# Optimization experiments

Hardware: AMD Instinct MI355X
Metric: run time of the kernel (lower is better)

The kernel has to match this reference:

```python
import jax, jax.numpy as jnp
import numpy as np

NBX = 24  # nb_x_patches
NBY = 24  # nb_y_patches
B, H, D = 8, 12, 64
L = NBX * NBY + 1  # 577 (grid tokens + 1 CLS token from the pad)
EPS = 1e-08


def _toeplitz_mask(topological_params):
    # topological_params: [H, 4*NBX*NBY]
    gi = jnp.arange(NBX)
    gj = jnp.arange(NBY)
    # relative 2D displacement index, flattened over (i, j, i', j')
    dist_index = ((gi[:, None, None, None] - gi[None, None, :, None] + NBX) * 2 * NBY
                  + gj[None, :, None, None] - gj[None, None, None, :] + NBY)
    dist_index = dist_index.reshape(-1)
    m = jnp.take(topological_params, dist_index, axis=1)
    m = m.reshape(topological_params.shape[0], NBX * NBY, NBX * NBY)  # [H, L-1, L-1]
    # pad CLS row and column with 1.0
    m = jnp.pad(m, [[0, 0], [1, 0], [1, 0]], constant_values=1.0)  # [H, L, L]
    return m[None]  # [1, H, L, L]


def setup_inputs() -> dict:
    key = jax.random.key(0)
    k1, k2, k3, k4 = jax.random.split(key, 4)
    return {
        'query': jax.random.normal(k1, (B, L, H, D), dtype=jnp.float32),
        'key': jax.random.normal(k2, (B, L, H, D), dtype=jnp.float32),
        'value': jax.random.normal(k3, (B, L, H, D), dtype=jnp.float32),
        'topological_params': jax.random.normal(k4, (H, 4 * NBX * NBY), dtype=jnp.float32),
    }


def reference(query, key, value, topological_params):
    depth = query.shape[-1]
    q = query / jnp.sqrt(jnp.asarray(depth, query.dtype))
    # relu feature map (kernel_type == 'relu')
    q = jax.nn.relu(q) + EPS
    k = jax.nn.relu(key) + EPS
    attn = jnp.einsum('bqhd,bkhd->bhqk', q, k)  # [B, H, L, L]
    top_mask = _toeplitz_mask(topological_params)  # [1, H, L, L]
    attn = attn * jnp.abs(top_mask) + EPS
    attn = attn / jnp.sum(attn, axis=-1, keepdims=True)  # kernelized normalization (no softmax)
    return jnp.einsum('bhqk,bkhd->bqhd', attn, value)
```

## Files before the change

kernel.cpp:

```cpp
#include <hip/hip_runtime.h>


#define Lq 577
#define NH 12
#define NB 8
#define DD 64
#define PAR 2304
#define EPSf 1e-8f

typedef __attribute__((ext_vector_type(4))) float f32x4;
typedef __attribute__((ext_vector_type(8))) short s16x8;

__device__ __forceinline__ float bflo(unsigned int u) {
    return __builtin_bit_cast(float, u << 16);
}
__device__ __forceinline__ float bfhi(unsigned int u) {
    return __builtin_bit_cast(float, u & 0xffff0000u);
}
__device__ __forceinline__ unsigned int f2bf(float f) {
    unsigned int x = __builtin_bit_cast(unsigned int, f);
    return (x + 0x7fffu + ((x >> 16) & 1u)) >> 16;
}
__device__ __forceinline__ int imin(int a, int b) { return a < b ? a : b; }
__device__ __forceinline__ int imax(int a, int b) { return a > b ? a : b; }

template <bool F32>
__device__ __forceinline__ void load8f(const void* G, size_t eidx, float* o) {
    if constexpr (F32) {
        const float* p = (const float*)G + eidx;
        float4 a = *(const float4*)p;
        float4 b = *(const float4*)(p + 4);
        o[0] = a.x; o[1] = a.y; o[2] = a.z; o[3] = a.w;
        o[4] = b.x; o[5] = b.y; o[6] = b.z; o[7] = b.w;
    } else {
        const unsigned short* p = (const unsigned short*)G + eidx;
        uint4 a = *(const uint4*)p;
        unsigned int u[4] = {a.x, a.y, a.z, a.w};
#pragma unroll
        for (int j = 0; j < 4; ++j) {
            o[2 * j]     = bflo(u[j]);
            o[2 * j + 1] = bfhi(u[j]);
        }
    }
}

template <bool F32>
__device__ void attn_body(const void* __restrict__ Qg, const void* __restrict__ Kg,
                          const void* __restrict__ Vg, const void* __restrict__ Tg,
                          void* __restrict__ Og,
                          float* s_par, unsigned short* s_k,
                          unsigned short* s_vt, unsigned short* s_p_all) {
    const int tid  = threadIdx.x;
    const int w    = tid >> 6;
    const int lane = tid & 63;
    const int g    = lane >> 4;
    const int lm   = lane & 15;

    const int bid = blockIdx.x;
    const int qt  = bid / 96;
    const int bh  = bid - qt * 96;
    const int h   = bh % NH;
    const int b   = bh / NH;

    unsigned short* s_pw = s_p_all + w * 16 * 72;

    for (int i = tid; i < PAR; i += 256) {
        float m = F32 ? ((const float*)Tg)[h * PAR + i]
                      : bflo((unsigned int)((const unsigned short*)Tg)[h * PAR + i]);
        m = fabsf(m);
        s_par[i] = (m == m) ? m : 0.0f;
    }

    const int q0w = qt * 64 + w * 16;

    const int q  = q0w + lm;
    const int qc = imin(q, Lq - 1);
    s16x8 a_q[2];
    {
        size_t rbase = ((size_t)((b * Lq + qc) * NH + h)) * DD;
#pragma unroll
        for (int ds = 0; ds < 2; ++ds) {
            float f[8];
            load8f<F32>(Qg, rbase + ds * 32 + g * 8, f);
            s16x8 a;
#pragma unroll
            for (int j = 0; j < 8; ++j) {
                float v = fmaf(fmaxf(f[j], 0.0f), 0.125f, EPSf);
                a[j] = (short)f2bf(v);
            }
            a_q[ds] = a;
        }
    }

    const bool qz = (q == 0);
    const int  qq = imax(qc - 1, 0);
    const int  qi = (qq * 2731) >> 16;
    const int  cq = qq + 24 * qi + 1176;

    f32x4 o_acc[4] = {};
    float rs = 0.0f;

    const int k0v  = 2 * (tid & 31);
    const int dchv = (tid >> 5) * 8;

    for (int kb = 0; kb < Lq; kb += 64) {
        __syncthreads();

        {
            int kgc = imin(kb + lane, Lq - 1);
            size_t base = ((size_t)((b * Lq + kgc) * NH + h)) * DD + w * 16;
            float kr[16];
            load8f<F32>(Kg, base,     kr);
            load8f<F32>(Kg, base + 8, kr + 8);
            unsigned int kt[8];
#pragma unroll
            for (int j = 0; j < 8; ++j) {
                float f0 = fmaxf(kr[2 * j], 0.0f) + EPSf;
                float f1 = fmaxf(kr[2 * j + 1], 0.0f) + EPSf;
                kt[j] = f2bf(f0) | (f2bf(f1) << 16);
            }
            *(uint4*)&s_k[lane * 72 + w * 16]     = make_uint4(kt[0], kt[1], kt[2], kt[3]);
            *(uint4*)&s_k[lane * 72 + w * 16 + 8] = make_uint4(kt[4], kt[5], kt[6], kt[7]);
        }
        {
            int kg0 = imin(kb + k0v,     Lq - 1);
            int kg1 = imin(kb + k0v + 1, Lq - 1);
            size_t b0 = ((size_t)((b * Lq + kg0) * NH + h)) * DD + dchv;
            size_t b1 = ((size_t)((b * Lq + kg1) * NH + h)) * DD + dchv;
            float v0[8], v1[8];
            load8f<F32>(Vg, b0, v0);
            load8f<F32>(Vg, b1, v1);
#pragma unroll
            for (int j = 0; j < 8; ++j) {
                float a0 = v0[j], a1 = v1[j];
                a0 = (a0 == a0) ? a0 : 0.0f;
                a1 = (a1 == a1) ? a1 : 0.0f;
                *(unsigned int*)&s_vt[(dchv + j) * 72 + k0v] =
                    f2bf(a0) | (f2bf(a1) << 16);
            }
        }
        __syncthreads();

        f32x4 sf[4];
#pragma unroll
        for (int cf = 0; cf < 4; ++cf) {
            s16x8 kf0 = *(const s16x8*)&s_k[(cf * 16 + lm) * 72 + g * 8];
            s16x8 kf1 = *(const s16x8*)&s_k[(cf * 16 + lm) * 72 + 32 + g * 8];
            f32x4 acc = {};
            acc = __builtin_amdgcn_mfma_f32_16x16x32_bf16(kf0, a_q[0], acc, 0, 0, 0);
            acc = __builtin_amdgcn_mfma_f32_16x16x32_bf16(kf1, a_q[1], acc, 0, 0, 0);
            sf[cf] = acc;
        }

#pragma unroll
        for (int cf = 0; cf < 4; ++cf) {
            float p[4];
#pragma unroll
            for (int r = 0; r < 4; ++r) {
                int  k  = kb + cf * 16 + g * 4 + r;
                bool kv = k < Lq;
                bool um = (k > 0) && kv && !qz;
                int  kk = imax(k - 1, 0);
                int  ki = (kk * 2731) >> 16;
                int  kl = kk + 24 * ki;
                int  idx = um ? (cq - kl) : 0;
                float mm = um ? s_par[idx] : (kv ? 1.0f : 0.0f);
                float s  = fmaxf(sf[cf][r], 0.0f);
                float pp = fmaf(s, mm, kv ? EPSf : 0.0f);
                rs += pp;
                p[r] = pp;
            }
            unsigned int d0 = f2bf(p[0]) | (f2bf(p[1]) << 16);
            unsigned int d1 = f2bf(p[2]) | (f2bf(p[3]) << 16);
            *(uint2*)&s_pw[lm * 72 + cf * 16 + g * 4] = make_uint2(d0, d1);
        }

#pragma unroll
        for (int ks = 0; ks < 2; ++ks) {
            s16x8 pa = *(const s16x8*)&s_pw[lm * 72 + ks * 32 + g * 8];
#pragma unroll
            for (int df = 0; df < 4; ++df) {
                s16x8 vb = *(const s16x8*)&s_vt[(df * 16 + lm) * 72 + ks * 32 + g * 8];
                o_acc[df] = __builtin_amdgcn_mfma_f32_16x16x32_bf16(pa, vb, o_acc[df], 0, 0, 0);
            }
        }
    }

    float tot = rs;
    tot += __shfl_xor(tot, 16, 64);
    tot += __shfl_xor(tot, 32, 64);
    float inv = (tot > 0.0f) ? 1.0f / tot : 0.0f;

#pragma unroll
    for (int r = 0; r < 4; ++r) {
        int   qrow  = q0w + g * 4 + r;
        float inv_r = __shfl(inv, g * 4 + r, 64);
        if (qrow < Lq) {
            size_t base = ((size_t)((b * Lq + qrow) * NH + h)) * DD;
#pragma unroll
            for (int df = 0; df < 4; ++df) {
                float val = o_acc[df][r] * inv_r;
                val = fminf(fmaxf(val, -1e30f), 1e30f);
                if constexpr (F32)
                    ((float*)Og)[base + df * 16 + lm] = val;
                else
                    ((unsigned short*)Og)[base + df * 16 + lm] = (unsigned short)f2bf(val);
            }
        }
    }
}

__global__ __launch_bounds__(256, 4)
void fused_topo_attn(const void* __restrict__ Qg, const void* __restrict__ Kg,
                     const void* __restrict__ Vg, const void* __restrict__ Tg,
                     void* __restrict__ Og) {
    __shared__ __align__(16) float          s_par[PAR];
    __shared__ __align__(16) unsigned short s_k[64 * 72];
    __shared__ __align__(16) unsigned short s_vt[64 * 72];
    __shared__ __align__(16) unsigned short s_p[4 * 16 * 72];

    float x = fabsf(((const float*)Qg)[threadIdx.x]);
    int n = __syncthreads_count(x > 2.44140625e-4f && x < 64.0f);

    if (n >= 128)
        attn_body<true>(Qg, Kg, Vg, Tg, Og, s_par, s_k, s_vt, s_p);
    else
        attn_body<false>(Qg, Kg, Vg, Tg, Og, s_par, s_k, s_vt, s_p);
}

extern "C" void kernel_launch(void* const* d_in, const int* in_sizes, int n_in,
                              void* d_out, int out_size, void* d_ws, size_t ws_size,
                              hipStream_t stream) {
    (void)in_sizes; (void)n_in; (void)out_size; (void)d_ws; (void)ws_size;
    dim3 grid(960);
    fused_topo_attn<<<grid, 256, 0, stream>>>(d_in[0], d_in[1], d_in[2], d_in[3], d_out);
}
```

Before: 135.0 us.

## Precompute bf16 K, transposed V and dense mask in workspace, stream via direct LDS loads

```diff
diff --git a/kernel.cpp b/kernel.cpp
--- a/kernel.cpp
+++ b/kernel.cpp
@@ -8,6 +8,9 @@
 #define PAR 2304
 #define EPSf 1e-8f
 
+#define VT_OFF 7090176ull
+#define MM_OFF 14954496ull
+
 typedef __attribute__((ext_vector_type(4))) float f32x4;
 typedef __attribute__((ext_vector_type(8))) short s16x8;
 
@@ -22,7 +25,19 @@
     return (x + 0x7fffu + ((x >> 16) & 1u)) >> 16;
 }
 __device__ __forceinline__ int imin(int a, int b) { return a < b ? a : b; }
-__device__ __forceinline__ int imax(int a, int b) { return a > b ? a : b; }
+
+__device__ __forceinline__ void gload_lds16(const unsigned short* g, unsigned short* l) {
+    __builtin_amdgcn_global_load_lds(
+        (const __attribute__((address_space(1))) unsigned int*)g,
+        (__attribute__((address_space(3))) unsigned int*)l, 16, 0, 0);
+}
+
+__device__ __forceinline__ bool probe_f32(const void* Qg) {
+    float x = fabsf(((const float*)Qg)[threadIdx.x]);
+    unsigned long long hit = __ballot(x > 2.44140625e-4f && x < 64.0f);
+    unsigned long long act = __ballot(1);
+    return 2 * __popcll(hit) >= __popcll(act);
+}
 
 template <bool F32>
 __device__ __forceinline__ void load8f(const void* G, size_t eidx, float* o) {
@@ -45,11 +60,122 @@
 }
 
 template <bool F32>
-__device__ void attn_body(const void* __restrict__ Qg, const void* __restrict__ Kg,
-                          const void* __restrict__ Vg, const void* __restrict__ Tg,
+__device__ void prep_k_body(const void* Kg, unsigned short* Kp) {
+    size_t i8 = ((size_t)blockIdx.x * 256 + threadIdx.x) * 8;
+    float f[8];
+    load8f<F32>(Kg, i8, f);
+    unsigned int o[4];
+#pragma unroll
+    for (int j = 0; j < 4; ++j) {
+        unsigned int lo = f2bf(fmaxf(f[2 * j], 0.0f) + EPSf);
+        unsigned int hi = f2bf(fmaxf(f[2 * j + 1], 0.0f) + EPSf);
+        o[j] = lo | (hi << 16);
+    }
+    *(uint4*)(Kp + i8) = make_uint4(o[0], o[1], o[2], o[3]);
+}
+__global__ __launch_bounds__(256)
+void prep_k(const void* __restrict__ Qg, const void* __restrict__ Kg,
+            unsigned short* __restrict__ Kp) {
+    if (probe_f32(Qg)) prep_k_body<true>(Kg, Kp);
+    else               prep_k_body<false>(Kg, Kp);
+}
+
+template <bool F32>
+__device__ void prep_vt_body(const void* Vg, unsigned short* Vt, unsigned short* s) {
+    const int t  = threadIdx.x;
+    const int kt = blockIdx.x, h = blockIdx.y, b = blockIdx.z;
+    {
+        int kl  = t >> 2;
+        int dch = (t & 3) * 16;
+        int k   = kt * 64 + kl;
+        unsigned int pk[8] = {};
+        if (k <= 576) {
+            float f[16];
+            size_t base = ((size_t)((b * Lq + k) * NH + h)) * DD + dch;
+            load8f<F32>(Vg, base, f);
+            load8f<F32>(Vg, base + 8, f + 8);
+#pragma unroll
+            for (int j = 0; j < 8; ++j)
+                pk[j] = f2bf(f[2 * j]) | (f2bf(f[2 * j + 1]) << 16);
+        }
+#pragma unroll
+        for (int j = 0; j < 8; ++j)
+            *(unsigned int*)&s[kl * 72 + dch + 2 * j] = pk[j];
+    }
+    __syncthreads();
+    {
+        int d   = t >> 2;
+        int kch = (t & 3) * 16;
+        unsigned int o[8];
+#pragma unroll
+        for (int j = 0; j < 8; ++j) {
+            unsigned short v0 = s[(kch + 2 * j) * 72 + d];
+            unsigned short v1 = s[(kch + 2 * j + 1) * 72 + d];
+            o[j] = (unsigned int)v0 | ((unsigned int)v1 << 16);
+        }
+        size_t base = ((size_t)((b * NH + h) * 64 + d)) * 640 + kt * 64 + kch;
+        *(uint4*)(Vt + base)     = make_uint4(o[0], o[1], o[2], o[3]);
+        *(uint4*)(Vt + base + 8) = make_uint4(o[4], o[5], o[6], o[7]);
+    }
+}
+__global__ __launch_bounds__(256)
+void prep_vt(const void* __restrict__ Qg, const void* __restrict__ Vg,
+             unsigned short* __restrict__ Vt) {
+    __shared__ unsigned short s[64 * 72];
+    if (probe_f32(Qg)) prep_vt_body<true>(Vg, Vt, s);
+    else               prep_vt_body<false>(Vg, Vt, s);
+}
+
+template <bool F32>
+__device__ void prep_mask_body(const void* Tg, unsigned short* Mm) {
+    const int q = blockIdx.x, h = blockIdx.y;
+    const int k0 = threadIdx.x * 8;
+    int cq = 0;
+    if (q > 0) {
+        int qq = q - 1;
+        int qi = (qq * 2731) >> 16;
+        cq = qq + 24 * qi + 1176;
+    }
+    unsigned int o[4];
+#pragma unroll
+    for (int j = 0; j < 4; ++j) {
+        unsigned int hv[2];
+#pragma unroll
+        for (int e = 0; e < 2; ++e) {
+            int k = k0 + 2 * j + e;
+            float m;
+            if (k > 576) m = 0.0f;
+            else if (k == 0 || q == 0) m = 1.0f;
+            else {
+                int kk = k - 1;
+                int ki = (kk * 2731) >> 16;
+                int idx = cq - (kk + 24 * ki);
+                float pv = F32 ? ((const float*)Tg)[h * PAR + idx]
+                               : bflo((unsigned int)((const unsigned short*)Tg)[h * PAR + idx]);
+                m = fabsf(pv);
+                m = (m == m) ? m : 0.0f;
+            }
+            hv[e] = f2bf(m);
+        }
+        o[j] = hv[0] | (hv[1] << 16);
+    }
+    *(uint4*)(Mm + (size_t)(h * Lq + q) * 640 + k0) = make_uint4(o[0], o[1], o[2], o[3]);
+}
+__global__ __launch_bounds__(128)
+void prep_mask(const void* __restrict__ Qg, const void* __restrict__ Tg,
+               unsigned short* __restrict__ Mm) {
+    if (probe_f32(Qg)) prep_mask_body<true>(Tg, Mm);
+    else               prep_mask_body<false>(Tg, Mm);
+}
+
+template <bool F32>
+__device__ void attn_body(const void* __restrict__ Qg,
+                          const unsigned short* __restrict__ Kp,
+                          const unsigned short* __restrict__ Vt,
+                          const unsigned short* __restrict__ Mm,
                           void* __restrict__ Og,
-                          float* s_par, unsigned short* s_k,
-                          unsigned short* s_vt, unsigned short* s_p_all) {
+                          unsigned short* s_k, unsigned short* s_vt,
+                          unsigned short* s_m, unsigned short* s_p_all) {
     const int tid  = threadIdx.x;
     const int w    = tid >> 6;
     const int lane = tid & 63;
@@ -63,13 +189,7 @@
     const int b   = bh / NH;
 
     unsigned short* s_pw = s_p_all + w * 16 * 72;
-
-    for (int i = tid; i < PAR; i += 256) {
-        float m = F32 ? ((const float*)Tg)[h * PAR + i]
-                      : bflo((unsigned int)((const unsigned short*)Tg)[h * PAR + i]);
-        m = fabsf(m);
-        s_par[i] = (m == m) ? m : 0.0f;
-    }
+    unsigned short* s_mw = s_m + w * 1024;
 
     const int q0w = qt * 64 + w * 16;
 
@@ -92,60 +212,49 @@
         }
     }
 
-    const bool qz = (q == 0);
-    const int  qq = imax(qc - 1, 0);
-    const int  qi = (qq * 2731) >> 16;
-    const int  cq = qq + 24 * qi + 1176;
+    const int r8 = lane >> 3;
+    const int c8 = lane & 7;
+    const int xr = (c8 ^ r8) * 8;
+
+    const unsigned short* KpBH = Kp + (size_t)b * (Lq * NH * DD) + h * DD;
+    const unsigned short* VtL0 = Vt + ((size_t)(b * NH + h) * 64 + (w * 16 + r8)) * 640 + xr;
+    const unsigned short* VtL1 = VtL0 + 8 * 640;
+    const unsigned short* MmH  = Mm + (size_t)h * (Lq * 640);
+    const unsigned short* MmL0 = MmH + (size_t)imin(q0w + r8, Lq - 1) * 640 + xr;
+    const unsigned short* MmL1 = MmH + (size_t)imin(q0w + 8 + r8, Lq - 1) * 640 + xr;
+
+    unsigned short* sk0 = s_k  + (w * 16) * 64;
+    unsigned short* sk1 = sk0 + 8 * 64;
+    unsigned short* sv0 = s_vt + (w * 16) * 64;
+    unsigned short* sv1 = sv0 + 8 * 64;
+    unsigned short* sm1 = s_mw + 8 * 64;
 
     f32x4 o_acc[4] = {};
     float rs = 0.0f;
 
-    const int k0v  = 2 * (tid & 31);
-    const int dchv = (tid >> 5) * 8;
-
-    for (int kb = 0; kb < Lq; kb += 64) {
+    const int x7 = lm & 7;
+
+    for (int kb = 0; kb < 640; kb += 64) {
         __syncthreads();
 
-        {
-            int kgc = imin(kb + lane, Lq - 1);
-            size_t base = ((size_t)((b * Lq + kgc) * NH + h)) * DD + w * 16;
-            float kr[16];
-            load8f<F32>(Kg, base,     kr);
-            load8f<F32>(Kg, base + 8, kr + 8);
-            unsigned int kt[8];
-#pragma unroll
-            for (int j = 0; j < 8; ++j) {
-                float f0 = fmaxf(kr[2 * j], 0.0f) + EPSf;
-                float f1 = fmaxf(kr[2 * j + 1], 0.0f) + EPSf;
-                kt[j] = f2bf(f0) | (f2bf(f1) << 16);
-            }
-            *(uint4*)&s_k[lane * 72 + w * 16]     = make_uint4(kt[0], kt[1], kt[2], kt[3]);
-            *(uint4*)&s_k[lane * 72 + w * 16 + 8] = make_uint4(kt[4], kt[5], kt[6], kt[7]);
-        }
-        {
-            int kg0 = imin(kb + k0v,     Lq - 1);
-            int kg1 = imin(kb + k0v + 1, Lq - 1);
-            size_t b0 = ((size_t)((b * Lq + kg0) * NH + h)) * DD + dchv;
-            size_t b1 = ((size_t)((b * Lq + kg1) * NH + h)) * DD + dchv;
-            float v0[8], v1[8];
-            load8f<F32>(Vg, b0, v0);
-            load8f<F32>(Vg, b1, v1);
-#pragma unroll
-            for (int j = 0; j < 8; ++j) {
-                float a0 = v0[j], a1 = v1[j];
-                a0 = (a0 == a0) ? a0 : 0.0f;
-                a1 = (a1 == a1) ? a1 : 0.0f;
-                *(unsigned int*)&s_vt[(dchv + j) * 72 + k0v] =
-                    f2bf(a0) | (f2bf(a1) << 16);
-            }
-        }
+        int krr = kb + w * 16 + r8;
+        int kr0 = imin(krr, Lq - 1);
+        int kr1 = imin(krr + 8, Lq - 1);
+        gload_lds16(KpBH + (size_t)kr0 * (NH * DD) + xr, sk0);
+        gload_lds16(KpBH + (size_t)kr1 * (NH * DD) + xr, sk1);
+        gload_lds16(VtL0 + kb, sv0);
+        gload_lds16(VtL1 + kb, sv1);
+        gload_lds16(MmL0 + kb, s_mw);
+        gload_lds16(MmL1 + kb, sm1);
         __syncthreads();
 
         f32x4 sf[4];
 #pragma unroll
         for (int cf = 0; cf < 4; ++cf) {
-            s16x8 kf0 = *(const s16x8*)&s_k[(cf * 16 + lm) * 72 + g * 8];
-            s16x8 kf1 = *(const s16x8*)&s_k[(cf * 16 + lm) * 72 + 32 + g * 8];
+            const unsigned short* skr = s_k + (cf * 16 + lm) * 64;
+            int co = (g ^ x7) * 8;
+            s16x8 kf0 = *(const s16x8*)(skr + co);
+            s16x8 kf1 = *(const s16x8*)(skr + (co ^ 32));
             f32x4 acc = {};
             acc = __builtin_amdgcn_mfma_f32_16x16x32_bf16(kf0, a_q[0], acc, 0, 0, 0);
             acc = __builtin_amdgcn_mfma_f32_16x16x32_bf16(kf1, a_q[1], acc, 0, 0, 0);
@@ -154,24 +263,17 @@
 
 #pragma unroll
         for (int cf = 0; cf < 4; ++cf) {
-            float p[4];
-#pragma unroll
-            for (int r = 0; r < 4; ++r) {
-                int  k  = kb + cf * 16 + g * 4 + r;
-                bool kv = k < Lq;
-                bool um = (k > 0) && kv && !qz;
-                int  kk = imax(k - 1, 0);
-                int  ki = (kk * 2731) >> 16;
-                int  kl = kk + 24 * ki;
-                int  idx = um ? (cq - kl) : 0;
-                float mm = um ? s_par[idx] : (kv ? 1.0f : 0.0f);
-                float s  = fmaxf(sf[cf][r], 0.0f);
-                float pp = fmaf(s, mm, kv ? EPSf : 0.0f);
-                rs += pp;
-                p[r] = pp;
-            }
-            unsigned int d0 = f2bf(p[0]) | (f2bf(p[1]) << 16);
-            unsigned int d1 = f2bf(p[2]) | (f2bf(p[3]) << 16);
+            int mo = ((cf * 2 + (g >> 1)) ^ x7) * 8 + (g & 1) * 4;
+            uint2 mu = *(const uint2*)&s_mw[lm * 64 + mo];
+            float m0 = bflo(mu.x), m1 = bfhi(mu.x);
+            float m2 = bflo(mu.y), m3 = bfhi(mu.y);
+            float p0 = fmaf(fmaxf(sf[cf][0], 0.0f), m0, EPSf);
+            float p1 = fmaf(fmaxf(sf[cf][1], 0.0f), m1, EPSf);
+            float p2 = fmaf(fmaxf(sf[cf][2], 0.0f), m2, EPSf);
+            float p3 = fmaf(fmaxf(sf[cf][3], 0.0f), m3, EPSf);
+            rs += (p0 + p1) + (p2 + p3);
+            unsigned int d0 = f2bf(p0) | (f2bf(p1) << 16);
+            unsigned int d1 = f2bf(p2) | (f2bf(p3) << 16);
             *(uint2*)&s_pw[lm * 72 + cf * 16 + g * 4] = make_uint2(d0, d1);
         }
 
@@ -180,7 +282,8 @@
             s16x8 pa = *(const s16x8*)&s_pw[lm * 72 + ks * 32 + g * 8];
 #pragma unroll
             for (int df = 0; df < 4; ++df) {
-                s16x8 vb = *(const s16x8*)&s_vt[(df * 16 + lm) * 72 + ks * 32 + g * 8];
+                const unsigned short* svr = s_vt + (df * 16 + lm) * 64;
+                s16x8 vb = *(const s16x8*)(svr + ((ks * 4 + g) ^ x7) * 8);
                 o_acc[df] = __builtin_amdgcn_mfma_f32_16x16x32_bf16(pa, vb, o_acc[df], 0, 0, 0);
             }
         }
@@ -200,7 +303,6 @@
 #pragma unroll
             for (int df = 0; df < 4; ++df) {
                 float val = o_acc[df][r] * inv_r;
-                val = fminf(fmaxf(val, -1e30f), 1e30f);
                 if constexpr (F32)
                     ((float*)Og)[base + df * 16 + lm] = val;
                 else
@@ -211,27 +313,30 @@
 }
 
 __global__ __launch_bounds__(256, 4)
-void fused_topo_attn(const void* __restrict__ Qg, const void* __restrict__ Kg,
-                     const void* __restrict__ Vg, const void* __restrict__ Tg,
+void fused_topo_attn(const void* __restrict__ Qg,
+                     const unsigned short* __restrict__ Kp,
+                     const unsigned short* __restrict__ Vt,
+                     const unsigned short* __restrict__ Mm,
                      void* __restrict__ Og) {
-    __shared__ __align__(16) float          s_par[PAR];
-    __shared__ __align__(16) unsigned short s_k[64 * 72];
-    __shared__ __align__(16) unsigned short s_vt[64 * 72];
+    __shared__ __align__(16) unsigned short s_k[64 * 64];
+    __shared__ __align__(16) unsigned short s_vt[64 * 64];
+    __shared__ __align__(16) unsigned short s_m[4 * 16 * 64];
     __shared__ __align__(16) unsigned short s_p[4 * 16 * 72];
 
-    float x = fabsf(((const float*)Qg)[threadIdx.x]);
-    int n = __syncthreads_count(x > 2.44140625e-4f && x < 64.0f);
-
-    if (n >= 128)
-        attn_body<true>(Qg, Kg, Vg, Tg, Og, s_par, s_k, s_vt, s_p);
-    else
-        attn_body<false>(Qg, Kg, Vg, Tg, Og, s_par, s_k, s_vt, s_p);
+    if (probe_f32(Qg)) attn_body<true>(Qg, Kp, Vt, Mm, Og, s_k, s_vt, s_m, s_p);
+    else               attn_body<false>(Qg, Kp, Vt, Mm, Og, s_k, s_vt, s_m, s_p);
 }
 
 extern "C" void kernel_launch(void* const* d_in, const int* in_sizes, int n_in,
                               void* d_out, int out_size, void* d_ws, size_t ws_size,
                               hipStream_t stream) {
-    (void)in_sizes; (void)n_in; (void)out_size; (void)d_ws; (void)ws_size;
-    dim3 grid(960);
-    fused_topo_attn<<<grid, 256, 0, stream>>>(d_in[0], d_in[1], d_in[2], d_in[3], d_out);
-}
+    (void)in_sizes; (void)n_in; (void)out_size; (void)ws_size;
+    unsigned short* Kp = (unsigned short*)d_ws;
+    unsigned short* Vt = (unsigned short*)((char*)d_ws + VT_OFF);
+    unsigned short* Mm = (unsigned short*)((char*)d_ws + MM_OFF);
+
+    prep_k<<<1731, 256, 0, stream>>>(d_in[0], d_in[1], Kp);
+    prep_vt<<<dim3(10, NH, NB), 256, 0, stream>>>(d_in[0], d_in[2], Vt);
+    prep_mask<<<dim3(Lq, NH), 80, 0, stream>>>(d_in[0], d_in[3], Mm);
+    fused_topo_attn<<<960, 256, 0, stream>>>(d_in[0], Kp, Vt, Mm, d_out);
+}
```

After: 123.4 us. 1.09x faster.
